# Performance work log

Measured on AMD Instinct MI355X. Metric: run time of the kernel, lower is better.

## Reference

```python
import jax, jax.numpy as jnp
import numpy as np
import math

B, T, L = 32, 512, 128
IN_C, D, H, NL = 512, 512, 8, 6
HD = D // H
DFF = 2 * D  # dim_feedforward = hidden_dim * 2 per __init__
V = 8000
BASE = 10000.0
EPS = 1e-5


def _rope_tables(n, hd):
    # standard RoPE: half-dim frequencies duplicated, matching precompute_rope_sin_cos
    inv = 1.0 / (BASE ** (jnp.arange(0, hd, 2, dtype=jnp.float32) / hd))
    ang = jnp.arange(n, dtype=jnp.float32)[:, None] * inv[None, :]  # [n, hd/2]
    cos = jnp.concatenate([jnp.cos(ang), jnp.cos(ang)], axis=-1)    # [n, hd]
    sin = jnp.concatenate([jnp.sin(ang), jnp.sin(ang)], axis=-1)
    return cos, sin


def _rot_half(x):
    x1, x2 = jnp.split(x, 2, axis=-1)
    return jnp.concatenate([-x2, x1], axis=-1)


def _ln(x, g, b):
    m = x.mean(-1, keepdims=True)
    v = jnp.mean((x - m) ** 2, axis=-1, keepdims=True)
    return (x - m) / jnp.sqrt(v + EPS) * g + b


def setup_inputs() -> dict:
    key = jax.random.key(0)
    ks = jax.random.split(key, 24)
    w = lambda k, s: jax.random.normal(k, s, jnp.float32) * 0.02
    z = lambda s: jnp.zeros(s, jnp.float32)
    o = lambda s: jnp.ones(s, jnp.float32)
    return {
        'encoder_features': jax.random.normal(ks[0], (B, T, IN_C), jnp.float32),
        'targets': jax.random.randint(ks[1], (B, L), 0, V),
        'emb': w(ks[2], (V, D)),
        'inp_w': w(ks[3], (D, IN_C)), 'inp_b': z((D,)),
        'out_w': w(ks[4], (V, D)), 'out_b': z((V,)),
        'qw': w(ks[5], (D, D)), 'qb': z((D,)),
        'kw': w(ks[6], (D, D)), 'kb': z((D,)),
        'vw': w(ks[7], (D, D)), 'vb': z((D,)),
        'ow': w(ks[8], (D, D)), 'ob': z((D,)),
        'mha_w': w(ks[9], (3 * D, D)), 'mha_b': z((3 * D,)),
        'mha_ow': w(ks[10], (D, D)), 'mha_ob': z((D,)),
        'w1': w(ks[11], (DFF, D)), 'b1': z((DFF,)),
        'w2': w(ks[12], (D, DFF)), 'b2': z((D,)),
        'ln1_g': o((D,)), 'ln1_b': z((D,)),
        'ln2_g': o((D,)), 'ln2_b': z((D,)),
        'ln3_g': o((D,)), 'ln3_b': z((D,)),
    }


def reference(encoder_features, targets, emb, inp_w, inp_b, out_w, out_b,
              qw, qb, kw, kb, vw, vb, ow, ob, mha_w, mha_b, mha_ow, mha_ob,
              w1, b1, w2, b2, ln1_g, ln1_b, ln2_g, ln2_b, ln3_g, ln3_b):
    memory = encoder_features @ inp_w.T + inp_b               # [B,T,D]
    tgt = emb[targets] * math.sqrt(D)                          # [B,L,D]
    mem_pad = jnp.abs(memory).sum(-1) == 0                     # [B,T] key padding mask
    causal = jnp.tril(jnp.ones((L, L), dtype=bool))
    cos, sin = _rope_tables(L, HD)                             # pos_ids = arange(0, L)
    scale = 1.0 / math.sqrt(HD)
    wq, wk, wv = jnp.split(mha_w, 3, axis=0)
    bq, bk, bv = jnp.split(mha_b, 3)

    for _ in range(NL):  # all layers share the same weights (ModuleList of one object)
        # --- self-attention with RoPE ---
        q = (tgt @ qw.T + qb).reshape(B, L, H, HD).transpose(0, 2, 1, 3)
        k = (tgt @ kw.T + kb).reshape(B, L, H, HD).transpose(0, 2, 1, 3)
        v = (tgt @ vw.T + vb).reshape(B, L, H, HD).transpose(0, 2, 1, 3)
        q = q * cos + _rot_half(q) * sin
        k = k * cos + _rot_half(k) * sin
        s = jnp.einsum('bhqd,bhkd->bhqk', q, k) * scale
        s = jnp.where(causal, s, -jnp.inf)
        a = jax.nn.softmax(s, axis=-1)
        o_sa = jnp.einsum('bhqk,bhkd->bhqd', a, v).transpose(0, 2, 1, 3).reshape(B, L, D)
        tgt = _ln(tgt + o_sa @ ow.T + ob, ln1_g, ln1_b)
        # --- cross-attention (nn.MultiheadAttention, batch_first) ---
        q2 = (tgt @ wq.T + bq).reshape(B, L, H, HD).transpose(0, 2, 1, 3)
        k2 = (memory @ wk.T + bk).reshape(B, T, H, HD).transpose(0, 2, 1, 3)
        v2 = (memory @ wv.T + bv).reshape(B, T, H, HD).transpose(0, 2, 1, 3)
        s2 = jnp.einsum('bhqd,bhkd->bhqk', q2, k2) * scale
        s2 = jnp.where(mem_pad[:, None, None, :], -jnp.inf, s2)
        a2 = jax.nn.softmax(s2, axis=-1)
        o_ca = jnp.einsum('bhqk,bhkd->bhqd', a2, v2).transpose(0, 2, 1, 3).reshape(B, L, D)
        tgt = _ln(tgt + o_ca @ mha_ow.T + mha_ob, ln2_g, ln2_b)
        # --- FFN (exact GELU, as nn.GELU default) ---
        ff = jax.nn.gelu(tgt @ w1.T + b1, approximate=False) @ w2.T + b2
        tgt = _ln(tgt + ff, ln3_g, ln3_b)

    logits = tgt @ out_w.T + out_b  # [B,L,V]
    return logits, tgt
```

## Files before the change

kernel.cpp:

```cpp
#include <hip/hip_runtime.h>
#include <hip/hip_bf16.h>

#define B_ 32
#define T_ 512
#define L_ 128
#define INC_ 512
#define D_ 512
#define H_ 8
#define HD_ 64
#define NL_ 6
#define DFF_ 1024
#define V_ 8000
#define LDSK 40
#define AST 72

typedef __bf16 bfr;
typedef __attribute__((ext_vector_type(8))) __bf16 bf16x8;
typedef __attribute__((ext_vector_type(4))) __bf16 bf16x4;
typedef __attribute__((ext_vector_type(4))) float f32x4;

struct ConvDesc { const float* src; bfr* dst; int n; int blk0; };
struct ConvTable { ConvDesc e[12]; int ne; };

__global__ void conv_many_kernel(ConvTable tab)
{
    int b = blockIdx.x;
    for (int i = 0; i < tab.ne; ++i) {
        const ConvDesc d = tab.e[i];
        int nb = d.n >> 11;
        if (b >= d.blk0 && b < d.blk0 + nb) {
            int g = ((b - d.blk0) * 256 + threadIdx.x) * 8;
            float4 v0 = *(const float4*)(d.src + g);
            float4 v1 = *(const float4*)(d.src + g + 4);
            bf16x8 o;
            o[0] = (bfr)v0.x; o[1] = (bfr)v0.y; o[2] = (bfr)v0.z; o[3] = (bfr)v0.w;
            o[4] = (bfr)v1.x; o[5] = (bfr)v1.y; o[6] = (bfr)v1.z; o[7] = (bfr)v1.w;
            *(bf16x8*)(d.dst + g) = o;
            return;
        }
    }
}

__global__ void copy3_kernel(const float* a, const float* b, const float* c, float* dst)
{
    int g = blockIdx.x * 256 + threadIdx.x;
    if (g < D_) dst[g] = a[g];
    else if (g < 2 * D_) dst[g] = b[g - D_];
    else if (g < 3 * D_) dst[g] = c[g - 2 * D_];
}

__device__ __forceinline__ void tile_map(int bid, int nbm, int nbn, int& pm, int& pn)
{
    int nwg = nbm * nbn;
    int q = nwg >> 3, r = nwg & 7;
    int xcd = bid & 7, idx = bid >> 3;
    int wgid = (xcd < r ? xcd * (q + 1) : r * (q + 1) + (xcd - r) * q) + idx;
    const int GROUP = 8;
    int per_group = GROUP * nbn;
    int gid = wgid / per_group;
    int first = gid * GROUP;
    int gsz = min(nbm - first, GROUP);
    int rem = wgid - gid * per_group;
    pm = first + rem % gsz;
    pn = rem / gsz;
}

template <int ACT, int OUT, int BM>
__global__ __launch_bounds__(256, 2) void gemm_ps(
    const bfr* __restrict__ Ahi,
    const bfr* __restrict__ Whi,
    const float* __restrict__ bias, float* __restrict__ Cf,
    bfr* __restrict__ Chi, int M, int N, int K)
{
    constexpr int MF = BM / 32;
    __shared__ bfr Ah_s[BM * LDSK];
    __shared__ bfr Wh_s[64 * LDSK];
    const int t = threadIdx.x;
    int pm, pn;
    tile_map(blockIdx.x, M / BM, N / 64, pm, pn);
    const int bm = pm * BM, bn = pn * 64;
    const int w = t >> 6, lane = t & 63;
    const int wm = w >> 1, wn = w & 1;
    const int fr = lane & 15, kq = lane >> 4;
    const int wr = t >> 2, wk = (t & 3) * 8;

    f32x4 acc[MF][2] = {};

    for (int k0 = 0; k0 < K; k0 += 32) {
        if constexpr (BM == 128) {
            const int ar = t >> 1, ah = (t & 1) * 16;
            const bfr* ap = Ahi + (size_t)(bm + ar) * K + (k0 + ah);
            *(bf16x8*)(Ah_s + ar * LDSK + ah) = *(const bf16x8*)ap;
            *(bf16x8*)(Ah_s + ar * LDSK + ah + 8) = *(const bf16x8*)(ap + 8);
        } else {
            const int ar = t >> 2, ah = (t & 3) * 8;
            *(bf16x8*)(Ah_s + ar * LDSK + ah) = *(const bf16x8*)(Ahi + (size_t)(bm + ar) * K + (k0 + ah));
        }
        *(bf16x8*)(Wh_s + wr * LDSK + wk) = *(const bf16x8*)(Whi + (size_t)(bn + wr) * K + (k0 + wk));
        __syncthreads();
        bf16x8 Afh[MF], Wfh[2];
#pragma unroll
        for (int i = 0; i < MF; ++i)
            Afh[i] = *(const bf16x8*)(Ah_s + (wm * (BM / 2) + i * 16 + fr) * LDSK + kq * 8);
#pragma unroll
        for (int j = 0; j < 2; ++j)
            Wfh[j] = *(const bf16x8*)(Wh_s + (wn * 32 + j * 16 + fr) * LDSK + kq * 8);
#pragma unroll
        for (int i = 0; i < MF; ++i)
#pragma unroll
            for (int j = 0; j < 2; ++j)
                acc[i][j] = __builtin_amdgcn_mfma_f32_16x16x32_bf16(Afh[i], Wfh[j], acc[i][j], 0, 0, 0);
        __syncthreads();
    }
#pragma unroll
    for (int i = 0; i < MF; ++i) {
        int row0 = bm + wm * (BM / 2) + i * 16 + (lane >> 4) * 4;
#pragma unroll
        for (int j = 0; j < 2; ++j) {
            int col = bn + wn * 32 + j * 16 + fr;
            float bj = bias[col];
#pragma unroll
            for (int r = 0; r < 4; ++r) {
                float v = acc[i][j][r] + bj;
                if (ACT == 1) v = 0.5f * v * (1.0f + erff(v * 0.70710678118654752f));
                size_t idx = (size_t)(row0 + r) * N + col;
                if (OUT == 0) Cf[idx] = v;
                else Chi[idx] = (bfr)v;
            }
        }
    }
}

template <int TK, int CAUSAL>
__global__ __launch_bounds__(512) void attn_wide(
    const bfr* __restrict__ Qg, int qstr,
    const bfr* __restrict__ Kg, const bfr* __restrict__ Vg, int kvstr,
    const int* __restrict__ pad,
    const float* __restrict__ cosT, const float* __restrict__ sinT,
    bfr* __restrict__ Ohi)
{
    __shared__ bfr Qs[128 * AST];
    __shared__ bfr Ks[64 * AST];
    __shared__ bfr VTs[64 * AST];
    __shared__ bfr Ps[128 * AST];
    const int bh = blockIdx.x;
    const int h = bh & 7, b = bh >> 3;
    const int t = threadIdx.x;
    const int w = t >> 6, lane = t & 63;
    const int l4 = lane & 15, hi4 = lane >> 4;
    const int qr0 = w * 16;

    {
        const int srow = t >> 2, ht = t & 3;
        if (CAUSAL) {
            const bfr* qp = Qg + (size_t)(b * L_ + srow) * qstr + h * HD_ + ht * 8;
            bf16x8 a = *(const bf16x8*)qp;
            bf16x8 bb = *(const bf16x8*)(qp + 32);
            bf16x8 o1, o2;
#pragma unroll
            for (int j = 0; j < 8; ++j) {
                float c = cosT[srow * 32 + ht * 8 + j], s = sinT[srow * 32 + ht * 8 + j];
                float x1 = (float)a[j], x2 = (float)bb[j];
                o1[j] = (bfr)(x1 * c - x2 * s);
                o2[j] = (bfr)(x2 * c + x1 * s);
            }
            *(bf16x8*)(Qs + srow * AST + ht * 8) = o1;
            *(bf16x8*)(Qs + srow * AST + ht * 8 + 32) = o2;
        } else {
            const bfr* qp = Qg + (size_t)(b * L_ + srow) * qstr + h * HD_ + ht * 16;
            *(bf16x8*)(Qs + srow * AST + ht * 16) = *(const bf16x8*)qp;
            *(bf16x8*)(Qs + srow * AST + ht * 16 + 8) = *(const bf16x8*)(qp + 8);
        }
    }

    f32x4 o_acc[4] = {};
    float m_run[4], l_run[4];
#pragma unroll
    for (int r = 0; r < 4; ++r) { m_run[r] = -1e30f; l_run[r] = 0.f; }

    for (int kt = 0; kt < TK / 64; ++kt) {
        __syncthreads();
        if (t < 256) {
            const int srow = t >> 2, ht = t & 3;
            int krow = kt * 64 + srow;
            if (CAUSAL) {
                const bfr* kp = Kg + (size_t)(b * TK + krow) * kvstr + h * HD_ + ht * 8;
                bf16x8 a = *(const bf16x8*)kp;
                bf16x8 bb = *(const bf16x8*)(kp + 32);
                bf16x8 o1, o2;
#pragma unroll
                for (int j = 0; j < 8; ++j) {
                    float c = cosT[krow * 32 + ht * 8 + j], s = sinT[krow * 32 + ht * 8 + j];
                    float x1 = (float)a[j], x2 = (float)bb[j];
                    o1[j] = (bfr)(x1 * c - x2 * s);
                    o2[j] = (bfr)(x2 * c + x1 * s);
                }
                *(bf16x8*)(Ks + srow * AST + ht * 8) = o1;
                *(bf16x8*)(Ks + srow * AST + ht * 8 + 32) = o2;
            } else {
                const bfr* kp = Kg + (size_t)(b * TK + krow) * kvstr + h * HD_ + ht * 16;
                *(bf16x8*)(Ks + srow * AST + ht * 16) = *(const bf16x8*)kp;
                *(bf16x8*)(Ks + srow * AST + ht * 16 + 8) = *(const bf16x8*)(kp + 8);
            }
        } else {
            const int tt = t - 256;
            const int srow = tt >> 2, ht = tt & 3;
            const bfr* vp = Vg + (size_t)(b * TK + kt * 64 + srow) * kvstr + h * HD_ + ht * 16;
            bf16x8 v0 = *(const bf16x8*)vp;
            bf16x8 v1 = *(const bf16x8*)(vp + 8);
#pragma unroll
            for (int i = 0; i < 8; ++i) VTs[(ht * 16 + i) * AST + srow] = v0[i];
#pragma unroll
            for (int i = 0; i < 8; ++i) VTs[(ht * 16 + 8 + i) * AST + srow] = v1[i];
        }
        __syncthreads();

        f32x4 s[4] = {};
#pragma unroll
        for (int kk = 0; kk < 64; kk += 32) {
            bf16x8 a = *(const bf16x8*)(Qs + (qr0 + l4) * AST + kk + hi4 * 8);
#pragma unroll
            for (int n = 0; n < 4; ++n) {
                bf16x8 bb = *(const bf16x8*)(Ks + (n * 16 + l4) * AST + kk + hi4 * 8);
                s[n] = __builtin_amdgcn_mfma_f32_16x16x32_bf16(a, bb, s[n], 0, 0, 0);
            }
        }
        float madd[4];
        if (!CAUSAL) {
#pragma unroll
            for (int n = 0; n < 4; ++n)
                madd[n] = pad[b * TK + kt * 64 + n * 16 + l4] ? -1e30f : 0.f;
        }
#pragma unroll
        for (int r = 0; r < 4; ++r) {
            int qrow = qr0 + hi4 * 4 + r;
            float sv[4];
#pragma unroll
            for (int n = 0; n < 4; ++n) {
                float x = s[n][r] * 0.125f;
                if (CAUSAL) {
                    int col = kt * 64 + n * 16 + l4;
                    if (col > qrow) x = -1e30f;
                } else x += madd[n];
                sv[n] = x;
            }
            float mx = fmaxf(fmaxf(sv[0], sv[1]), fmaxf(sv[2], sv[3]));
#pragma unroll
            for (int off = 1; off < 16; off <<= 1) mx = fmaxf(mx, __shfl_xor(mx, off));
            float mnew = fmaxf(m_run[r], mx);
            float alpha = expf(m_run[r] - mnew);
            float pv[4], psum = 0.f;
#pragma unroll
            for (int n = 0; n < 4; ++n) { pv[n] = expf(sv[n] - mnew); psum += pv[n]; }
#pragma unroll
            for (int off = 1; off < 16; off <<= 1) psum += __shfl_xor(psum, off);
            l_run[r] = l_run[r] * alpha + psum;
            m_run[r] = mnew;
#pragma unroll
            for (int n = 0; n < 4; ++n) o_acc[n][r] *= alpha;
#pragma unroll
            for (int n = 0; n < 4; ++n)
                Ps[(qr0 + hi4 * 4 + r) * AST + n * 16 + l4] = (bfr)pv[n];
        }
#pragma unroll
        for (int kk = 0; kk < 64; kk += 32) {
            bf16x8 pa = *(const bf16x8*)(Ps + (qr0 + l4) * AST + kk + hi4 * 8);
#pragma unroll
            for (int n = 0; n < 4; ++n) {
                bf16x8 vb = *(const bf16x8*)(VTs + (n * 16 + l4) * AST + kk + hi4 * 8);
                o_acc[n] = __builtin_amdgcn_mfma_f32_16x16x32_bf16(pa, vb, o_acc[n], 0, 0, 0);
            }
        }
    }
#pragma unroll
    for (int r = 0; r < 4; ++r) {
        float inv = 1.0f / l_run[r];
        int qrow = qr0 + hi4 * 4 + r;
#pragma unroll
        for (int n = 0; n < 4; ++n)
            Ohi[(size_t)(b * L_ + qrow) * D_ + h * HD_ + n * 16 + l4] = (bfr)(o_acc[n][r] * inv);
    }
}

__global__ void rope_tables_kernel(float* __restrict__ cosT, float* __restrict__ sinT)
{
    int gid = blockIdx.x * blockDim.x + threadIdx.x;
    if (gid >= L_ * 32) return;
    int l = gid >> 5, i = gid & 31;
    float inv = powf(10000.0f, -(float)(2 * i) / (float)HD_);
    float ang = (float)l * inv;
    cosT[gid] = cosf(ang);
    sinT[gid] = sinf(ang);
}

__global__ void embed_kernel(const int* __restrict__ targets, const float* __restrict__ emb,
                             float* __restrict__ tgt, bfr* __restrict__ thi)
{
    int gid = blockIdx.x * blockDim.x + threadIdx.x;
    if (gid >= B_ * L_ * D_) return;
    int d = gid & (D_ - 1);
    int r = gid >> 9;
    int tok = targets[r];
    float x = emb[(size_t)tok * D_ + d] * 22.62741699796952f;
    tgt[gid] = x;
    thi[gid] = (bfr)x;
}

__global__ void pad_kernel(const bfr* __restrict__ mem, int* __restrict__ pad)
{
    int gid = blockIdx.x * blockDim.x + threadIdx.x;
    if (gid >= B_ * T_) return;
    const bfr* p = mem + (size_t)gid * D_;
    float s = 0.f;
    for (int d0 = 0; d0 < D_; d0 += 8) {
        bf16x8 v = *(const bf16x8*)(p + d0);
#pragma unroll
        for (int j = 0; j < 8; ++j) s += fabsf((float)v[j]);
    }
    pad[gid] = (s == 0.0f) ? 1 : 0;
}

__global__ __launch_bounds__(128) void ln_residual_kernel(
    const float* __restrict__ tgt, const bfr* __restrict__ delta,
    const float* __restrict__ g, const float* __restrict__ bb,
    float* __restrict__ yout, bfr* __restrict__ thi)
{
    const int row = blockIdx.x;
    const int t = threadIdx.x;
    __shared__ float rbuf[128];
    size_t base = (size_t)row * D_ + t * 4;
    float4 x = *(const float4*)(tgt + base);
    bf16x4 dl = *(const bf16x4*)(delta + base);
    x.x += (float)dl[0]; x.y += (float)dl[1]; x.z += (float)dl[2]; x.w += (float)dl[3];
    rbuf[t] = x.x + x.y + x.z + x.w;
    __syncthreads();
    for (int off = 64; off > 0; off >>= 1) { if (t < off) rbuf[t] += rbuf[t + off]; __syncthreads(); }
    float mean = rbuf[0] * (1.0f / D_);
    __syncthreads();
    float4 d4 = {x.x - mean, x.y - mean, x.z - mean, x.w - mean};
    rbuf[t] = d4.x * d4.x + d4.y * d4.y + d4.z * d4.z + d4.w * d4.w;
    __syncthreads();
    for (int off = 64; off > 0; off >>= 1) { if (t < off) rbuf[t] += rbuf[t + off]; __syncthreads(); }
    float inv = 1.0f / sqrtf(rbuf[0] * (1.0f / D_) + 1e-5f);
    float4 g4 = *(const float4*)(g + t * 4);
    float4 b4 = *(const float4*)(bb + t * 4);
    float4 y = {d4.x * inv * g4.x + b4.x, d4.y * inv * g4.y + b4.y,
                d4.z * inv * g4.z + b4.z, d4.w * inv * g4.w + b4.w};
    *(float4*)(yout + base) = y;
    bf16x4 h4 = {(bfr)y.x, (bfr)y.y, (bfr)y.z, (bfr)y.w};
    *(bf16x4*)(thi + base) = h4;
}

__global__ void fillf_kernel(float* p, float v, size_t n)
{
    size_t gid = (size_t)blockIdx.x * 256 + threadIdx.x;
    if (gid < n) p[gid] = v;
}

extern "C" void kernel_launch(void* const* d_in, const int* in_sizes, int n_in,
                              void* d_out, int out_size, void* d_ws, size_t ws_size,
                              hipStream_t stream)
{
    const float* enc    = (const float*)d_in[0];
    const int*   tg     = (const int*)d_in[1];
    const float* emb    = (const float*)d_in[2];
    const float* inp_w  = (const float*)d_in[3];
    const float* inp_b  = (const float*)d_in[4];
    const float* out_w  = (const float*)d_in[5];
    const float* out_b  = (const float*)d_in[6];
    const float* qw     = (const float*)d_in[7];
    const float* qb     = (const float*)d_in[8];
    const float* kw     = (const float*)d_in[9];
    const float* kb     = (const float*)d_in[10];
    const float* vw     = (const float*)d_in[11];
    const float* vb     = (const float*)d_in[12];
    const float* ow     = (const float*)d_in[13];
    const float* ob     = (const float*)d_in[14];
    const float* mha_w  = (const float*)d_in[15];
    const float* mha_b  = (const float*)d_in[16];
    const float* mha_ow = (const float*)d_in[17];
    const float* mha_ob = (const float*)d_in[18];
    const float* w1     = (const float*)d_in[19];
    const float* b1     = (const float*)d_in[20];
    const float* w2     = (const float*)d_in[21];
    const float* b2     = (const float*)d_in[22];
    const float* ln1g   = (const float*)d_in[23];
    const float* ln1b   = (const float*)d_in[24];
    const float* ln2g   = (const float*)d_in[25];
    const float* ln2b   = (const float*)d_in[26];
    const float* ln3g   = (const float*)d_in[27];
    const float* ln3b   = (const float*)d_in[28];

    const int BL = B_ * L_;
    const int BT = B_ * T_;
    const size_t N_LOGITS = (size_t)BL * V_;
    const int D2 = D_ * D_;

    const size_t WS_NEEDED =
        (size_t)BT * 1024 * sizeof(bfr)
        + (size_t)BL * D_ * sizeof(float)
        + (size_t)BL * D_ * sizeof(bfr)
        + (size_t)2 * L_ * 32 * sizeof(float) + (size_t)BT * sizeof(int)
        + (size_t)V_ * D_ * sizeof(bfr);
    if (ws_size < WS_NEEDED) {
        fillf_kernel<<<((size_t)out_size + 255) / 256, 256, 0, stream>>>((float*)d_out, 0.f, (size_t)out_size);
        return;
    }
    bfr*   f_KVb = (bfr*)d_ws;
    float* f_tgt = (float*)(f_KVb + (size_t)BT * 1024);
    bfr*   tgt_hi = (bfr*)(f_tgt + (size_t)BL * D_);
    float* f_cos = (float*)(tgt_hi + (size_t)BL * D_);
    float* f_sin = f_cos + (size_t)L_ * 32;
    int*   f_pad = (int*)(f_sin + (size_t)L_ * 32);
    bfr*   ow_hi = (bfr*)(f_pad + BT);

    bfr* wp = (bfr*)d_out;
    bfr* qkvw_hi = wp;  wp += 3 * D2;
    bfr* inp_hi  = wp;  wp += D2;
    bfr* mha_hi  = wp;  wp += 3 * D2;
    bfr* o_hi    = wp;  wp += D2;
    bfr* mo_hi   = wp;  wp += D2;
    bfr* w1_hi   = wp;  wp += DFF_ * D_;
    bfr* w2_hi   = wp;  wp += D_ * DFF_;
    float* f_qkvb = (float*)wp;
    float* lr    = f_qkvb + 3 * D_;
    bfr*   t2_b  = (bfr*)lr;
    bfr*   qkv   = t2_b + (size_t)BL * D_;
    bfr*   qcr   = qkv + (size_t)BL * 3 * D_;
    bfr*   t1_hi = qcr + (size_t)BL * D_;
    bfr*   ffh_hi = t1_hi + (size_t)BL * D_;
    bfr*   enc_hi = (bfr*)lr;
    bfr*   mem_hi = enc_hi + (size_t)BT * D_;

    {
        ConvTable tab{};
        int blk = 0, ne = 0;
        auto add = [&](const float* s, bfr* d, int n) {
            tab.e[ne] = {s, d, n, blk};
            blk += n >> 11;
            ++ne;
        };
        add(qw, qkvw_hi, D2);
        add(kw, qkvw_hi + D2, D2);
        add(vw, qkvw_hi + 2 * D2, D2);
        add(inp_w, inp_hi, D2);
        add(mha_w, mha_hi, 3 * D2);
        add(ow, o_hi, D2);
        add(mha_ow, mo_hi, D2);
        add(w1, w1_hi, DFF_ * D_);
        add(w2, w2_hi, D_ * DFF_);
        add(out_w, ow_hi, V_ * D_);
        add(enc, enc_hi, BT * D_);
        tab.ne = ne;
        conv_many_kernel<<<blk, 256, 0, stream>>>(tab);
    }
    copy3_kernel<<<6, 256, 0, stream>>>(qb, kb, vb, f_qkvb);

    rope_tables_kernel<<<(L_ * 32 + 255) / 256, 256, 0, stream>>>(f_cos, f_sin);
    embed_kernel<<<(BL * D_ + 255) / 256, 256, 0, stream>>>(tg, emb, f_tgt, tgt_hi);

    gemm_ps<0, 1, 128><<<(BT / 128) * (D_ / 64), 256, 0, stream>>>(enc_hi, inp_hi, inp_b, nullptr, mem_hi, BT, D_, INC_);
    pad_kernel<<<(BT + 255) / 256, 256, 0, stream>>>(mem_hi, f_pad);
    gemm_ps<0, 1, 128><<<(BT / 128) * (1024 / 64), 256, 0, stream>>>(mem_hi, mha_hi + (size_t)D2, mha_b + D_, nullptr, f_KVb, BT, 1024, D_);

    float* o_logits = (float*)d_out;
    float* o_tgt = o_logits + N_LOGITS;

    for (int layer = 0; layer < NL_; ++layer) {
        gemm_ps<0, 1, 64><<<(BL / 64) * (3 * D_ / 64), 256, 0, stream>>>(tgt_hi, qkvw_hi, f_qkvb, nullptr, qkv, BL, 3 * D_, D_);
        attn_wide<L_, 1><<<B_ * H_, 512, 0, stream>>>(qkv, 3 * D_, qkv + D_, qkv + 2 * D_, 3 * D_, nullptr, f_cos, f_sin, t1_hi);
        gemm_ps<0, 1, 64><<<(BL / 64) * (D_ / 64), 256, 0, stream>>>(t1_hi, o_hi, ob, nullptr, t2_b, BL, D_, D_);
        ln_residual_kernel<<<BL, 128, 0, stream>>>(f_tgt, t2_b, ln1g, ln1b, f_tgt, tgt_hi);
        gemm_ps<0, 1, 64><<<(BL / 64) * (D_ / 64), 256, 0, stream>>>(tgt_hi, mha_hi, mha_b, nullptr, qcr, BL, D_, D_);
        attn_wide<T_, 0><<<B_ * H_, 512, 0, stream>>>(qcr, D_, f_KVb, f_KVb + D_, 1024, f_pad, nullptr, nullptr, t1_hi);
        gemm_ps<0, 1, 64><<<(BL / 64) * (D_ / 64), 256, 0, stream>>>(t1_hi, mo_hi, mha_ob, nullptr, t2_b, BL, D_, D_);
        ln_residual_kernel<<<BL, 128, 0, stream>>>(f_tgt, t2_b, ln2g, ln2b, f_tgt, tgt_hi);
        gemm_ps<1, 1, 64><<<(BL / 64) * (DFF_ / 64), 256, 0, stream>>>(tgt_hi, w1_hi, b1, nullptr, ffh_hi, BL, DFF_, D_);
        gemm_ps<0, 1, 64><<<(BL / 64) * (D_ / 64), 256, 0, stream>>>(ffh_hi, w2_hi, b2, nullptr, t2_b, BL, D_, DFF_);
        float* yout = (layer == NL_ - 1) ? o_tgt : f_tgt;
        ln_residual_kernel<<<BL, 128, 0, stream>>>(f_tgt, t2_b, ln3g, ln3b, yout, tgt_hi);
    }

    gemm_ps<0, 0, 128><<<(BL / 128) * (V_ / 64), 256, 0, stream>>>(tgt_hi, ow_hi, out_b, o_logits, nullptr, BL, V_, D_);
}
```

Baseline: 945.0 us.

## Double-buffer K/V tiles in attention and skip fully masked causal tiles

```diff
diff --git a/kernel.cpp b/kernel.cpp
--- a/kernel.cpp
+++ b/kernel.cpp
@@ -140,8 +140,8 @@
     bfr* __restrict__ Ohi)
 {
     __shared__ bfr Qs[128 * AST];
-    __shared__ bfr Ks[64 * AST];
-    __shared__ bfr VTs[64 * AST];
+    __shared__ bfr Ks[2][64 * AST];
+    __shared__ bfr VTs[2][64 * AST];
     __shared__ bfr Ps[128 * AST];
     const int bh = blockIdx.x;
     const int h = bh & 7, b = bh >> 3;
@@ -149,128 +149,178 @@
     const int w = t >> 6, lane = t & 63;
     const int l4 = lane & 15, hi4 = lane >> 4;
     const int qr0 = w * 16;
+    const bool kstage = t < 256;
+    const int srow = (t & 255) >> 2, ht = t & 3;
 
     {
-        const int srow = t >> 2, ht = t & 3;
+        const int qrow = t >> 2, qh = t & 3;
         if (CAUSAL) {
-            const bfr* qp = Qg + (size_t)(b * L_ + srow) * qstr + h * HD_ + ht * 8;
+            const bfr* qp = Qg + (size_t)(b * L_ + qrow) * qstr + h * HD_ + qh * 8;
             bf16x8 a = *(const bf16x8*)qp;
             bf16x8 bb = *(const bf16x8*)(qp + 32);
             bf16x8 o1, o2;
 #pragma unroll
             for (int j = 0; j < 8; ++j) {
-                float c = cosT[srow * 32 + ht * 8 + j], s = sinT[srow * 32 + ht * 8 + j];
+                float c = cosT[qrow * 32 + qh * 8 + j], s = sinT[qrow * 32 + qh * 8 + j];
                 float x1 = (float)a[j], x2 = (float)bb[j];
                 o1[j] = (bfr)(x1 * c - x2 * s);
                 o2[j] = (bfr)(x2 * c + x1 * s);
             }
-            *(bf16x8*)(Qs + srow * AST + ht * 8) = o1;
-            *(bf16x8*)(Qs + srow * AST + ht * 8 + 32) = o2;
+            *(bf16x8*)(Qs + qrow * AST + qh * 8) = o1;
+            *(bf16x8*)(Qs + qrow * AST + qh * 8 + 32) = o2;
         } else {
-            const bfr* qp = Qg + (size_t)(b * L_ + srow) * qstr + h * HD_ + ht * 16;
-            *(bf16x8*)(Qs + srow * AST + ht * 16) = *(const bf16x8*)qp;
-            *(bf16x8*)(Qs + srow * AST + ht * 16 + 8) = *(const bf16x8*)(qp + 8);
-        }
-    }
+            const bfr* qp = Qg + (size_t)(b * L_ + qrow) * qstr + h * HD_ + qh * 16;
+            *(bf16x8*)(Qs + qrow * AST + qh * 16) = *(const bf16x8*)qp;
+            *(bf16x8*)(Qs + qrow * AST + qh * 16 + 8) = *(const bf16x8*)(qp + 8);
+        }
+    }
+
+    const int NT = TK / 64;
+    bf16x8 r0, r1;
+
+    {
+        int nrow = srow;
+        if (kstage) {
+            if (CAUSAL) {
+                const bfr* kp = Kg + (size_t)(b * TK + nrow) * kvstr + h * HD_ + ht * 8;
+                bf16x8 a = *(const bf16x8*)kp;
+                bf16x8 bb = *(const bf16x8*)(kp + 32);
+#pragma unroll
+                for (int j = 0; j < 8; ++j) {
+                    float c = cosT[nrow * 32 + ht * 8 + j], s = sinT[nrow * 32 + ht * 8 + j];
+                    float x1 = (float)a[j], x2 = (float)bb[j];
+                    r0[j] = (bfr)(x1 * c - x2 * s);
+                    r1[j] = (bfr)(x2 * c + x1 * s);
+                }
+                *(bf16x8*)(Ks[0] + srow * AST + ht * 8) = r0;
+                *(bf16x8*)(Ks[0] + srow * AST + ht * 8 + 32) = r1;
+            } else {
+                const bfr* kp = Kg + (size_t)(b * TK + nrow) * kvstr + h * HD_ + ht * 16;
+                *(bf16x8*)(Ks[0] + srow * AST + ht * 16) = *(const bf16x8*)kp;
+                *(bf16x8*)(Ks[0] + srow * AST + ht * 16 + 8) = *(const bf16x8*)(kp + 8);
+            }
+        } else {
+            const bfr* vp = Vg + (size_t)(b * TK + nrow) * kvstr + h * HD_ + ht * 16;
+            bf16x8 v0 = *(const bf16x8*)vp;
+            bf16x8 v1 = *(const bf16x8*)(vp + 8);
+#pragma unroll
+            for (int i = 0; i < 8; ++i) VTs[0][(ht * 16 + i) * AST + srow] = v0[i];
+#pragma unroll
+            for (int i = 0; i < 8; ++i) VTs[0][(ht * 16 + 8 + i) * AST + srow] = v1[i];
+        }
+    }
+    __syncthreads();
 
     f32x4 o_acc[4] = {};
     float m_run[4], l_run[4];
 #pragma unroll
     for (int r = 0; r < 4; ++r) { m_run[r] = -1e30f; l_run[r] = 0.f; }
 
-    for (int kt = 0; kt < TK / 64; ++kt) {
+    for (int kt = 0; kt < NT; ++kt) {
+        const int cur = kt & 1;
+        const bool have_next = (kt + 1 < NT);
+        if (have_next) {
+            int nrow = (kt + 1) * 64 + srow;
+            if (kstage) {
+                if (CAUSAL) {
+                    const bfr* kp = Kg + (size_t)(b * TK + nrow) * kvstr + h * HD_ + ht * 8;
+                    bf16x8 a = *(const bf16x8*)kp;
+                    bf16x8 bb = *(const bf16x8*)(kp + 32);
+#pragma unroll
+                    for (int j = 0; j < 8; ++j) {
+                        float c = cosT[nrow * 32 + ht * 8 + j], s = sinT[nrow * 32 + ht * 8 + j];
+                        float x1 = (float)a[j], x2 = (float)bb[j];
+                        r0[j] = (bfr)(x1 * c - x2 * s);
+                        r1[j] = (bfr)(x2 * c + x1 * s);
+                    }
+                } else {
+                    const bfr* kp = Kg + (size_t)(b * TK + nrow) * kvstr + h * HD_ + ht * 16;
+                    r0 = *(const bf16x8*)kp;
+                    r1 = *(const bf16x8*)(kp + 8);
+                }
+            } else {
+                const bfr* vp = Vg + (size_t)(b * TK + nrow) * kvstr + h * HD_ + ht * 16;
+                r0 = *(const bf16x8*)vp;
+                r1 = *(const bf16x8*)(vp + 8);
+            }
+        }
+        const bool active = !CAUSAL || (kt * 64 <= qr0 + 15);
+        if (active) {
+            f32x4 s[4] = {};
+#pragma unroll
+            for (int kk = 0; kk < 64; kk += 32) {
+                bf16x8 a = *(const bf16x8*)(Qs + (qr0 + l4) * AST + kk + hi4 * 8);
+#pragma unroll
+                for (int n = 0; n < 4; ++n) {
+                    bf16x8 bb = *(const bf16x8*)(Ks[cur] + (n * 16 + l4) * AST + kk + hi4 * 8);
+                    s[n] = __builtin_amdgcn_mfma_f32_16x16x32_bf16(a, bb, s[n], 0, 0, 0);
+                }
+            }
+            float madd[4];
+            if (!CAUSAL) {
+#pragma unroll
+                for (int n = 0; n < 4; ++n)
+                    madd[n] = pad[b * TK + kt * 64 + n * 16 + l4] ? -1e30f : 0.f;
+            }
+#pragma unroll
+            for (int r = 0; r < 4; ++r) {
+                int qrow = qr0 + hi4 * 4 + r;
+                float sv[4];
+#pragma unroll
+                for (int n = 0; n < 4; ++n) {
+                    float x = s[n][r] * 0.125f;
+                    if (CAUSAL) {
+                        int col = kt * 64 + n * 16 + l4;
+                        if (col > qrow) x = -1e30f;
+                    } else x += madd[n];
+                    sv[n] = x;
+                }
+                float mx = fmaxf(fmaxf(sv[0], sv[1]), fmaxf(sv[2], sv[3]));
+#pragma unroll
+                for (int off = 1; off < 16; off <<= 1) mx = fmaxf(mx, __shfl_xor(mx, off));
+                float mnew = fmaxf(m_run[r], mx);
+                float alpha = expf(m_run[r] - mnew);
+                float pv[4], psum = 0.f;
+#pragma unroll
+                for (int n = 0; n < 4; ++n) { pv[n] = expf(sv[n] - mnew); psum += pv[n]; }
+#pragma unroll
+                for (int off = 1; off < 16; off <<= 1) psum += __shfl_xor(psum, off);
+                l_run[r] = l_run[r] * alpha + psum;
+                m_run[r] = mnew;
+#pragma unroll
+                for (int n = 0; n < 4; ++n) o_acc[n][r] *= alpha;
+#pragma unroll
+                for (int n = 0; n < 4; ++n)
+                    Ps[(qr0 + hi4 * 4 + r) * AST + n * 16 + l4] = (bfr)pv[n];
+            }
+#pragma unroll
+            for (int kk = 0; kk < 64; kk += 32) {
+                bf16x8 pa = *(const bf16x8*)(Ps + (qr0 + l4) * AST + kk + hi4 * 8);
+#pragma unroll
+                for (int n = 0; n < 4; ++n) {
+                    bf16x8 vb = *(const bf16x8*)(VTs[cur] + (n * 16 + l4) * AST + kk + hi4 * 8);
+                    o_acc[n] = __builtin_amdgcn_mfma_f32_16x16x32_bf16(pa, vb, o_acc[n], 0, 0, 0);
+                }
+            }
+        }
+        if (have_next) {
+            const int nxt = cur ^ 1;
+            if (kstage) {
+                if (CAUSAL) {
+                    *(bf16x8*)(Ks[nxt] + srow * AST + ht * 8) = r0;
+                    *(bf16x8*)(Ks[nxt] + srow * AST + ht * 8 + 32) = r1;
+                } else {
+                    *(bf16x8*)(Ks[nxt] + srow * AST + ht * 16) = r0;
+                    *(bf16x8*)(Ks[nxt] + srow * AST + ht * 16 + 8) = r1;
+                }
+            } else {
+#pragma unroll
+                for (int i = 0; i < 8; ++i) VTs[nxt][(ht * 16 + i) * AST + srow] = r0[i];
+#pragma unroll
+                for (int i = 0; i < 8; ++i) VTs[nxt][(ht * 16 + 8 + i) * AST + srow] = r1[i];
+            }
+        }
         __syncthreads();
-        if (t < 256) {
-            const int srow = t >> 2, ht = t & 3;
-            int krow = kt * 64 + srow;
-            if (CAUSAL) {
-                const bfr* kp = Kg + (size_t)(b * TK + krow) * kvstr + h * HD_ + ht * 8;
-                bf16x8 a = *(const bf16x8*)kp;
-                bf16x8 bb = *(const bf16x8*)(kp + 32);
-                bf16x8 o1, o2;
-#pragma unroll
-                for (int j = 0; j < 8; ++j) {
-                    float c = cosT[krow * 32 + ht * 8 + j], s = sinT[krow * 32 + ht * 8 + j];
-                    float x1 = (float)a[j], x2 = (float)bb[j];
-                    o1[j] = (bfr)(x1 * c - x2 * s);
-                    o2[j] = (bfr)(x2 * c + x1 * s);
-                }
-                *(bf16x8*)(Ks + srow * AST + ht * 8) = o1;
-                *(bf16x8*)(Ks + srow * AST + ht * 8 + 32) = o2;
-            } else {
-                const bfr* kp = Kg + (size_t)(b * TK + krow) * kvstr + h * HD_ + ht * 16;
-                *(bf16x8*)(Ks + srow * AST + ht * 16) = *(const bf16x8*)kp;
-                *(bf16x8*)(Ks + srow * AST + ht * 16 + 8) = *(const bf16x8*)(kp + 8);
-            }
-        } else {
-            const int tt = t - 256;
-            const int srow = tt >> 2, ht = tt & 3;
-            const bfr* vp = Vg + (size_t)(b * TK + kt * 64 + srow) * kvstr + h * HD_ + ht * 16;
-            bf16x8 v0 = *(const bf16x8*)vp;
-            bf16x8 v1 = *(const bf16x8*)(vp + 8);
-#pragma unroll
-            for (int i = 0; i < 8; ++i) VTs[(ht * 16 + i) * AST + srow] = v0[i];
-#pragma unroll
-            for (int i = 0; i < 8; ++i) VTs[(ht * 16 + 8 + i) * AST + srow] = v1[i];
-        }
-        __syncthreads();
-
-        f32x4 s[4] = {};
-#pragma unroll
-        for (int kk = 0; kk < 64; kk += 32) {
-            bf16x8 a = *(const bf16x8*)(Qs + (qr0 + l4) * AST + kk + hi4 * 8);
-#pragma unroll
-            for (int n = 0; n < 4; ++n) {
-                bf16x8 bb = *(const bf16x8*)(Ks + (n * 16 + l4) * AST + kk + hi4 * 8);
-                s[n] = __builtin_amdgcn_mfma_f32_16x16x32_bf16(a, bb, s[n], 0, 0, 0);
-            }
-        }
-        float madd[4];
-        if (!CAUSAL) {
-#pragma unroll
-            for (int n = 0; n < 4; ++n)
-                madd[n] = pad[b * TK + kt * 64 + n * 16 + l4] ? -1e30f : 0.f;
-        }
-#pragma unroll
-        for (int r = 0; r < 4; ++r) {
-            int qrow = qr0 + hi4 * 4 + r;
-            float sv[4];
-#pragma unroll
-            for (int n = 0; n < 4; ++n) {
-                float x = s[n][r] * 0.125f;
-                if (CAUSAL) {
-                    int col = kt * 64 + n * 16 + l4;
-                    if (col > qrow) x = -1e30f;
-                } else x += madd[n];
-                sv[n] = x;
-            }
-            float mx = fmaxf(fmaxf(sv[0], sv[1]), fmaxf(sv[2], sv[3]));
-#pragma unroll
-            for (int off = 1; off < 16; off <<= 1) mx = fmaxf(mx, __shfl_xor(mx, off));
-            float mnew = fmaxf(m_run[r], mx);
-            float alpha = expf(m_run[r] - mnew);
-            float pv[4], psum = 0.f;
-#pragma unroll
-            for (int n = 0; n < 4; ++n) { pv[n] = expf(sv[n] - mnew); psum += pv[n]; }
-#pragma unroll
-            for (int off = 1; off < 16; off <<= 1) psum += __shfl_xor(psum, off);
-            l_run[r] = l_run[r] * alpha + psum;
-            m_run[r] = mnew;
-#pragma unroll
-            for (int n = 0; n < 4; ++n) o_acc[n][r] *= alpha;
-#pragma unroll
-            for (int n = 0; n < 4; ++n)
-                Ps[(qr0 + hi4 * 4 + r) * AST + n * 16 + l4] = (bfr)pv[n];
-        }
-#pragma unroll
-        for (int kk = 0; kk < 64; kk += 32) {
-            bf16x8 pa = *(const bf16x8*)(Ps + (qr0 + l4) * AST + kk + hi4 * 8);
-#pragma unroll
-            for (int n = 0; n < 4; ++n) {
-                bf16x8 vb = *(const bf16x8*)(VTs + (n * 16 + l4) * AST + kk + hi4 * 8);
-                o_acc[n] = __builtin_amdgcn_mfma_f32_16x16x32_bf16(pa, vb, o_acc[n], 0, 0, 0);
-            }
-        }
     }
 #pragma unroll
     for (int r = 0; r < 4; ++r) {
```

After: 914.7 us. -3.2%, faster.
